# Performance work log

Measured on AMD Instinct MI355X. Metric: run time of the kernel, lower is better.

The kernel has to match this reference:

```python
import jax, jax.numpy as jnp
import numpy as np

N_NODES = 50000
N_EDGES = 1600000
DIM = 128
HEADS = 8
HEAD_DIM = DIM // HEADS


def setup_inputs() -> dict:
    key = jax.random.key(0)
    ks = jax.random.split(key, 12)
    s = 1.0 / np.sqrt(DIM)
    return {
        "x": jax.random.normal(ks[0], (N_NODES, DIM), dtype=jnp.float32),
        "src": jax.random.randint(ks[1], (N_EDGES,), 0, N_NODES, dtype=jnp.int32),
        "dst": jax.random.randint(ks[2], (N_EDGES,), 0, N_NODES, dtype=jnp.int32),
        "Wq": jax.random.uniform(ks[3], (DIM, DIM), jnp.float32, -s, s),
        "bq": jax.random.uniform(ks[4], (DIM,), jnp.float32, -s, s),
        "Wk": jax.random.uniform(ks[5], (DIM, DIM), jnp.float32, -s, s),
        "bk": jax.random.uniform(ks[6], (DIM,), jnp.float32, -s, s),
        "Wv": jax.random.uniform(ks[7], (DIM, DIM), jnp.float32, -s, s),
        "bv": jax.random.uniform(ks[8], (DIM,), jnp.float32, -s, s),
        "Wo": jax.random.uniform(ks[9], (DIM, DIM), jnp.float32, -s, s),
        "bo": jax.random.uniform(ks[10], (DIM,), jnp.float32, -s, s),
    }


def reference(x, src, dst, Wq, bq, Wk, bk, Wv, bv, Wo, bo):
    # Linear projections (torch Linear: x @ W.T + b), split into heads
    q = (x @ Wq.T + bq).reshape(-1, HEADS, HEAD_DIM)  # [N, H, Dh]
    k = (x @ Wk.T + bk).reshape(-1, HEADS, HEAD_DIM)
    v = (x @ Wv.T + bv).reshape(-1, HEADS, HEAD_DIM)

    # u_dot_v: per-edge dot of q[src] and k[dst] per head -> [E, H]
    scores = jnp.einsum("ehd,ehd->eh", q[src], k[dst]) / np.sqrt(HEAD_DIM).astype(np.float32)

    # edge_softmax: softmax over edges grouped by destination node
    m = jax.ops.segment_max(scores, dst, num_segments=N_NODES)  # [N, H]
    e = jnp.exp(scores - m[dst])
    z = jax.ops.segment_sum(e, dst, num_segments=N_NODES)  # [N, H]
    probs = e / z[dst]  # [E, H]

    # u_mul_e_sum: scatter-add of v[src] * probs into dst -> [N, H, Dh]
    msg = v[src] * probs[:, :, None]
    agg = jax.ops.segment_sum(msg, dst, num_segments=N_NODES)

    out = agg.reshape(-1, DIM) @ Wo.T + bo  # dropout p=0.0 -> identity
    return out
```

## Files before the change

### kernel.cpp

```cpp
#include <hip/hip_runtime.h>
#include <hip/hip_bf16.h>
#include <math.h>

#define N_NODES 50000
#define N_EDGES 1600000
#define NBUCK 256
#define NBUCK_ACTIVE ((N_NODES + 255) / 256)
#define P1_BLOCKS ((N_EDGES + 4095) / 4096)
#define CAP 9216
#define QKV_BLOCKS ((N_NODES + 63) / 64)

typedef short bf16x8 __attribute__((ext_vector_type(8)));
typedef float f32x4 __attribute__((ext_vector_type(4)));

#define SC2 0.3606737602222409f
#define MNEG -1.0e30f

static __device__ __forceinline__ unsigned short f2bf(float f) {
  unsigned int b = __float_as_uint(f);
  unsigned int r = (b + 0x7FFFu + ((b >> 16) & 1u)) >> 16;
  return (unsigned short)r;
}
static __device__ __forceinline__ float bf_lo(unsigned int u) {
  return __uint_as_float(u << 16);
}
static __device__ __forceinline__ float bf_hi(unsigned int u) {
  return __uint_as_float(u & 0xFFFF0000u);
}

__global__ __launch_bounds__(256) void bucket_partition(
    const int* __restrict__ src, const int* __restrict__ dst,
    int* __restrict__ bcursor, unsigned int* __restrict__ packed,
    const float* __restrict__ Wq, const float* __restrict__ Wk,
    const float* __restrict__ Wv, const float* __restrict__ Wo,
    unsigned short* __restrict__ wb) {
  const int t = threadIdx.x;
  if (blockIdx.x < 64) {
    int idx = blockIdx.x * 256 + t;
    wb[idx] = f2bf(Wq[idx]);
    wb[16384 + idx] = f2bf(Wk[idx]);
    wb[32768 + idx] = f2bf(Wv[idx]);
    wb[49152 + idx] = f2bf(Wo[idx]);
  }

  __shared__ int h[NBUCK];
  __shared__ int sd[NBUCK];
  __shared__ int lofs[NBUCK];
  __shared__ int gbase[NBUCK];
  __shared__ unsigned int stage[4096];
  __shared__ unsigned short sbin[4096];

  h[t] = 0;
  __syncthreads();
  const int ebase = blockIdx.x * 4096;
  const int count = min(4096, N_EDGES - ebase);
  const int base4 = blockIdx.x * 1024;
  unsigned int val[16];
  int binrank[16];
#pragma unroll
  for (int i = 0; i < 4; ++i) {
    int i4 = base4 + i * 256 + t;
    if (i4 < N_EDGES / 4) {
      int4 s4 = ((const int4*)src)[i4];
      int4 d4 = ((const int4*)dst)[i4];
      int ss[4] = {s4.x, s4.y, s4.z, s4.w};
      int dd[4] = {d4.x, d4.y, d4.z, d4.w};
#pragma unroll
      for (int j = 0; j < 4; ++j) {
        val[i * 4 + j] = ((unsigned)dd[j] << 16) | (unsigned)ss[j];
        int bin = dd[j] >> 8;
        int r = atomicAdd(&h[bin], 1);
        binrank[i * 4 + j] = (bin << 16) | r;
      }
    } else {
#pragma unroll
      for (int j = 0; j < 4; ++j) binrank[i * 4 + j] = -1;
    }
  }
  __syncthreads();
  const int own = h[t];
  if (own > 0) gbase[t] = atomicAdd(&bcursor[t], own);
  sd[t] = own;
  __syncthreads();
  for (int d = 1; d < NBUCK; d <<= 1) {
    int v = (t >= d) ? sd[t - d] : 0;
    __syncthreads();
    sd[t] += v;
    __syncthreads();
  }
  lofs[t] = sd[t] - own;
  __syncthreads();
#pragma unroll
  for (int i = 0; i < 16; ++i) {
    if (binrank[i] >= 0) {
      int bin = binrank[i] >> 16;
      int r = binrank[i] & 0xFFFF;
      int slot = lofs[bin] + r;
      stage[slot] = val[i];
      sbin[slot] = (unsigned short)bin;
    }
  }
  __syncthreads();
  for (int j = t; j < count; j += 256) {
    int b = sbin[j];
    packed[(size_t)b * CAP + gbase[b] + (j - lofs[b])] = stage[j];
  }
}

__global__ __launch_bounds__(256) void qkv_and_finalize(
    const float* __restrict__ x, const unsigned short* __restrict__ wb,
    const float* __restrict__ bq, const float* __restrict__ bk,
    const float* __restrict__ bv,
    unsigned short* __restrict__ qrec, unsigned short* __restrict__ kb,
    unsigned short* __restrict__ vrec,
    const unsigned int* __restrict__ packed, const int* __restrict__ bcursor,
    int* __restrict__ ebeg, int* __restrict__ eend,
    unsigned short* __restrict__ ssrc, int nrows) {
  __shared__ __align__(16) unsigned short sbuf[64 * 136];
  const int tid = threadIdx.x;

  if (blockIdx.x < QKV_BLOCKS) {
    const int w = tid >> 6;
    const int lane = tid & 63;
    const int lr = lane & 15;
    const int kg = lane >> 4;
    const int rowbase = blockIdx.x * 64;
    const int arow = min(rowbase + w * 16 + lr, nrows - 1);

    bf16x8 af[4];
    const float* xr = x + (size_t)arow * 128;
#pragma unroll
    for (int ksub = 0; ksub < 4; ++ksub) {
      const int k0 = ksub * 32 + kg * 8;
      float4 f0 = *(const float4*)(xr + k0);
      float4 f1 = *(const float4*)(xr + k0 + 4);
      af[ksub][0] = (short)f2bf(f0.x);
      af[ksub][1] = (short)f2bf(f0.y);
      af[ksub][2] = (short)f2bf(f0.z);
      af[ksub][3] = (short)f2bf(f0.w);
      af[ksub][4] = (short)f2bf(f1.x);
      af[ksub][5] = (short)f2bf(f1.y);
      af[ksub][6] = (short)f2bf(f1.z);
      af[ksub][7] = (short)f2bf(f1.w);
    }

    for (int p = 0; p < 3; ++p) {
      const unsigned short* wp = wb + p * 16384;
      const float* bias = (p == 0) ? bq : (p == 1) ? bk : bv;
      unsigned short* gout = (p == 0) ? qrec : (p == 1) ? kb : vrec;
      f32x4 acc[8];
#pragma unroll
      for (int nt = 0; nt < 8; ++nt) {
        float b = bias[nt * 16 + lr];
        acc[nt] = (f32x4){b, b, b, b};
      }
#pragma unroll
      for (int ksub = 0; ksub < 4; ++ksub) {
#pragma unroll
        for (int nt = 0; nt < 8; ++nt) {
          bf16x8 bfr = *(const bf16x8*)(wp + (size_t)(nt * 16 + lr) * 128 +
                                        ksub * 32 + kg * 8);
          acc[nt] = __builtin_amdgcn_mfma_f32_16x16x32_bf16(af[ksub], bfr,
                                                            acc[nt], 0, 0, 0);
        }
      }
      __syncthreads();
#pragma unroll
      for (int nt = 0; nt < 8; ++nt) {
        int col = nt * 16 + lr;
#pragma unroll
        for (int r = 0; r < 4; ++r)
          sbuf[(w * 16 + kg * 4 + r) * 136 + col] = f2bf(acc[nt][r]);
      }
      __syncthreads();
#pragma unroll
      for (int i = 0; i < 4; ++i) {
        int idx = i * 256 + tid;
        int lrow = idx >> 4;
        int u16o = (idx & 15) * 8;
        int grow = rowbase + lrow;
        if (grow < nrows)
          *(uint4*)(gout + (size_t)grow * 128 + u16o) =
              *(const uint4*)&sbuf[lrow * 136 + u16o];
      }
    }
  } else {
    int* cnt = (int*)sbuf;
    int* sd = cnt + NBUCK;
    int* cur = sd + NBUCK;
    const int t = tid;
    const int b = blockIdx.x - QKV_BLOCKS;
    const int beg = b * CAP;
    const int n_in_bucket = min(bcursor[b], CAP);
    cnt[t] = 0;
    __syncthreads();
    for (int e = t; e < n_in_bucket; e += 256)
      atomicAdd(&cnt[(packed[beg + e] >> 16) & 255], 1);
    __syncthreads();
    const int own = cnt[t];
    sd[t] = own;
    __syncthreads();
    for (int d = 1; d < NBUCK; d <<= 1) {
      int v = (t >= d) ? sd[t - d] : 0;
      __syncthreads();
      sd[t] += v;
      __syncthreads();
    }
    const int excl = sd[t] - own;
    cur[t] = excl;
    const int node = b * 256 + t;
    if (node < N_NODES) {
      ebeg[node] = beg + excl;
      eend[node] = beg + excl + own;
    }
    __syncthreads();
    for (int e = t; e < n_in_bucket; e += 256) {
      unsigned int p = packed[beg + e];
      int local = (p >> 16) & 255;
      int r = atomicAdd(&cur[local], 1);
      ssrc[beg + r] = (unsigned short)(p & 0xFFFFu);
    }
  }
}

__global__ __launch_bounds__(256, 4) void edge_agg_out(
    const unsigned short* __restrict__ qrec, const unsigned short* __restrict__ vrec,
    const unsigned short* __restrict__ kb,
    const int* __restrict__ ebeg, const int* __restrict__ eend,
    const unsigned short* __restrict__ ssrc,
    const unsigned short* __restrict__ wo, const float* __restrict__ bo,
    float* __restrict__ out) {
  __shared__ __align__(16) unsigned short aggs[16 * 136];
  const int wid = threadIdx.x >> 6;
  const int lane = threadIdx.x & 63;
  const int l16 = lane & 15;
  const int qq = lane >> 4;
  const int loff = l16 * 8;
  const int nbase = blockIdx.x * 16;

#define DOT8(t0)                                                       \
  (bf_lo(t0.x) * k0 + bf_hi(t0.x) * k1 + bf_lo(t0.y) * k2 +            \
   bf_hi(t0.y) * k3 + bf_lo(t0.z) * k4 + bf_hi(t0.z) * k5 +            \
   bf_lo(t0.w) * k6 + bf_hi(t0.w) * k7)

#define ACC8(pe, tv)                        \
  a0 = fmaf(pe, bf_lo(tv.x), a0);           \
  a1 = fmaf(pe, bf_hi(tv.x), a1);           \
  a2 = fmaf(pe, bf_lo(tv.y), a2);           \
  a3 = fmaf(pe, bf_hi(tv.y), a3);           \
  a4 = fmaf(pe, bf_lo(tv.z), a4);           \
  a5 = fmaf(pe, bf_hi(tv.z), a5);           \
  a6 = fmaf(pe, bf_lo(tv.w), a6);           \
  a7 = fmaf(pe, bf_hi(tv.w), a7)

  for (int i = 0; i < 4; ++i) {
    const int n = nbase + wid * 4 + i;
    const uint4 ku = *(const uint4*)(kb + (size_t)n * 128 + loff);
    const float k0 = bf_lo(ku.x), k1 = bf_hi(ku.x);
    const float k2 = bf_lo(ku.y), k3 = bf_hi(ku.y);
    const float k4 = bf_lo(ku.z), k5 = bf_hi(ku.z);
    const float k6 = bf_lo(ku.w), k7 = bf_hi(ku.w);

    const int start = ebeg[n];
    const int end = eend[n];

    float zz = 0.0f;
    float a0 = 0, a1 = 0, a2 = 0, a3 = 0, a4 = 0, a5 = 0, a6 = 0, a7 = 0;

    int base = start;
    for (; base + 16 <= end; base += 16) {
      int sA = ssrc[base + qq];
      int sB = ssrc[base + 4 + qq];
      int sC = ssrc[base + 8 + qq];
      int sD = ssrc[base + 12 + qq];
      const uint4 qA = *(const uint4*)(qrec + ((size_t)sA << 7) + loff);
      const uint4 vA = *(const uint4*)(vrec + ((size_t)sA << 7) + loff);
      const uint4 qB = *(const uint4*)(qrec + ((size_t)sB << 7) + loff);
      const uint4 vB = *(const uint4*)(vrec + ((size_t)sB << 7) + loff);
      const uint4 qC = *(const uint4*)(qrec + ((size_t)sC << 7) + loff);
      const uint4 vC = *(const uint4*)(vrec + ((size_t)sC << 7) + loff);
      const uint4 qD = *(const uint4*)(qrec + ((size_t)sD << 7) + loff);
      const uint4 vD = *(const uint4*)(vrec + ((size_t)sD << 7) + loff);

      float pA = DOT8(qA);
      float pB = DOT8(qB);
      float pC = DOT8(qC);
      float pD = DOT8(qD);
      pA += __shfl_xor(pA, 1);
      pB += __shfl_xor(pB, 1);
      pC += __shfl_xor(pC, 1);
      pD += __shfl_xor(pD, 1);
      float peA = __builtin_amdgcn_exp2f(pA * SC2);
      float peB = __builtin_amdgcn_exp2f(pB * SC2);
      float peC = __builtin_amdgcn_exp2f(pC * SC2);
      float peD = __builtin_amdgcn_exp2f(pD * SC2);
      zz += (peA + peB) + (peC + peD);
      ACC8(peA, vA);
      ACC8(peB, vB);
      ACC8(peC, vC);
      ACC8(peD, vD);
    }
    for (; base < end; base += 4) {
      int idx = base + qq;
      bool valid = idx < end;
      int s = ssrc[valid ? idx : end - 1];
      const uint4 q0 = *(const uint4*)(qrec + ((size_t)s << 7) + loff);
      const uint4 v0 = *(const uint4*)(vrec + ((size_t)s << 7) + loff);
      float p = DOT8(q0);
      p += __shfl_xor(p, 1);
      float pe = __builtin_amdgcn_exp2f(valid ? p * SC2 : MNEG);
      zz += pe;
      ACC8(pe, v0);
    }

#pragma unroll
    for (int off = 16; off <= 32; off <<= 1) {
      zz += __shfl_xor(zz, off);
      a0 += __shfl_xor(a0, off);
      a1 += __shfl_xor(a1, off);
      a2 += __shfl_xor(a2, off);
      a3 += __shfl_xor(a3, off);
      a4 += __shfl_xor(a4, off);
      a5 += __shfl_xor(a5, off);
      a6 += __shfl_xor(a6, off);
      a7 += __shfl_xor(a7, off);
    }
    float inv = (zz > 0.0f) ? 1.0f / zz : 0.0f;

    if (qq == 0) {
      unsigned short o[8] = {f2bf(a0 * inv), f2bf(a1 * inv), f2bf(a2 * inv),
                             f2bf(a3 * inv), f2bf(a4 * inv), f2bf(a5 * inv),
                             f2bf(a6 * inv), f2bf(a7 * inv)};
      *(uint4*)&aggs[(wid * 4 + i) * 136 + loff] = *(const uint4*)o;
    }
  }
#undef DOT8
#undef ACC8

  __syncthreads();

  bf16x8 af[4];
#pragma unroll
  for (int ksub = 0; ksub < 4; ++ksub)
    af[ksub] = *(const bf16x8*)&aggs[l16 * 136 + ksub * 32 + qq * 8];

  f32x4 acc[2];
#pragma unroll
  for (int j = 0; j < 2; ++j) {
    int nt = wid * 2 + j;
    float b = bo[nt * 16 + l16];
    acc[j] = (f32x4){b, b, b, b};
  }
#pragma unroll
  for (int ksub = 0; ksub < 4; ++ksub) {
#pragma unroll
    for (int j = 0; j < 2; ++j) {
      int nt = wid * 2 + j;
      bf16x8 bfr = *(const bf16x8*)(wo + (size_t)(nt * 16 + l16) * 128 +
                                    ksub * 32 + qq * 8);
      acc[j] =
          __builtin_amdgcn_mfma_f32_16x16x32_bf16(af[ksub], bfr, acc[j], 0, 0, 0);
    }
  }
#pragma unroll
  for (int j = 0; j < 2; ++j) {
    int col = (wid * 2 + j) * 16 + l16;
#pragma unroll
    for (int r = 0; r < 4; ++r) {
      int grow = nbase + qq * 4 + r;
      out[(size_t)grow * 128 + col] = acc[j][r];
    }
  }
}

extern "C" void kernel_launch(void* const* d_in, const int* in_sizes, int n_in,
                              void* d_out, int out_size, void* d_ws, size_t ws_size,
                              hipStream_t stream) {
  const float* x  = (const float*)d_in[0];
  const int* src  = (const int*)d_in[1];
  const int* dst  = (const int*)d_in[2];
  const float* Wq = (const float*)d_in[3];
  const float* bq = (const float*)d_in[4];
  const float* Wk = (const float*)d_in[5];
  const float* bk = (const float*)d_in[6];
  const float* Wv = (const float*)d_in[7];
  const float* bv = (const float*)d_in[8];
  const float* Wo = (const float*)d_in[9];
  const float* bo = (const float*)d_in[10];
  float* out = (float*)d_out;

  char* ws = (char*)d_ws;
  size_t off = 0;
  auto carve = [&](size_t bytes) {
    size_t r = off;
    off = (off + bytes + 255) & ~(size_t)255;
    return r;
  };
  unsigned short* qrec = (unsigned short*)(ws + carve((size_t)N_NODES * 256));
  unsigned short* vrec = (unsigned short*)(ws + carve((size_t)N_NODES * 256));
  unsigned short* kb   = (unsigned short*)(ws + carve((size_t)N_NODES * 256));
  unsigned int* packed = (unsigned int*)(ws + carve((size_t)NBUCK * CAP * 4));
  unsigned short* ssrc = (unsigned short*)(ws + carve((size_t)NBUCK * CAP * 2));
  int* ebeg    = (int*)(ws + carve((size_t)N_NODES * sizeof(int)));
  int* eend    = (int*)(ws + carve((size_t)N_NODES * sizeof(int)));
  int* bcursor = (int*)(ws + carve(NBUCK * sizeof(int)));
  unsigned short* wb = (unsigned short*)(ws + carve((size_t)4 * 128 * 128 * 2));

  hipMemsetAsync(bcursor, 0, NBUCK * sizeof(int), stream);

  bucket_partition<<<P1_BLOCKS, 256, 0, stream>>>(src, dst, bcursor, packed,
                                                  Wq, Wk, Wv, Wo, wb);

  qkv_and_finalize<<<QKV_BLOCKS + NBUCK_ACTIVE, 256, 0, stream>>>(
      x, wb, bq, bk, bv, qrec, kb, vrec, packed, bcursor, ebeg, eend, ssrc,
      N_NODES);

  edge_agg_out<<<N_NODES / 16, 256, 0, stream>>>(qrec, vrec, kb, ebeg, eend,
                                                 ssrc, wb + 3 * 16384, bo, out);
}
```

Before: 191.5 us.

## Co-schedule QKV projection with edge bucketing; split bucket finalize into own kernel

Moves the edge bucket partition into the same launch as the QKV projection, so the projection blocks and partition blocks run concurrently. The bucket finalize stage becomes a separate small kernel. The QKV blocks now read the fp32 weights directly and convert them to bf16 on the fly, removing the dependency on a pre-converted weight buffer; only Wo is still pre-converted. The cost is redundant weight conversion in every QKV block, more fp32 weight loads, and larger shared memory for the combined kernel.

```diff
diff --git a/kernel.cpp b/kernel.cpp
--- a/kernel.cpp
+++ b/kernel.cpp
@@ -27,99 +27,33 @@
 static __device__ __forceinline__ float bf_hi(unsigned int u) {
   return __uint_as_float(u & 0xFFFF0000u);
 }
-
-__global__ __launch_bounds__(256) void bucket_partition(
+static __device__ __forceinline__ bf16x8 cvt8(const float* p) {
+  float4 w0 = *(const float4*)p;
+  float4 w1 = *(const float4*)(p + 4);
+  bf16x8 r;
+  r[0] = (short)f2bf(w0.x); r[1] = (short)f2bf(w0.y);
+  r[2] = (short)f2bf(w0.z); r[3] = (short)f2bf(w0.w);
+  r[4] = (short)f2bf(w1.x); r[5] = (short)f2bf(w1.y);
+  r[6] = (short)f2bf(w1.z); r[7] = (short)f2bf(w1.w);
+  return r;
+}
+
+__global__ __launch_bounds__(256) void qkv_and_partition(
+    const float* __restrict__ x,
+    const float* __restrict__ Wq, const float* __restrict__ bq,
+    const float* __restrict__ Wk, const float* __restrict__ bk,
+    const float* __restrict__ Wv, const float* __restrict__ bv,
+    const float* __restrict__ Wo,
+    unsigned short* __restrict__ qrec, unsigned short* __restrict__ kb,
+    unsigned short* __restrict__ vrec,
     const int* __restrict__ src, const int* __restrict__ dst,
     int* __restrict__ bcursor, unsigned int* __restrict__ packed,
-    const float* __restrict__ Wq, const float* __restrict__ Wk,
-    const float* __restrict__ Wv, const float* __restrict__ Wo,
-    unsigned short* __restrict__ wb) {
-  const int t = threadIdx.x;
-  if (blockIdx.x < 64) {
-    int idx = blockIdx.x * 256 + t;
-    wb[idx] = f2bf(Wq[idx]);
-    wb[16384 + idx] = f2bf(Wk[idx]);
-    wb[32768 + idx] = f2bf(Wv[idx]);
-    wb[49152 + idx] = f2bf(Wo[idx]);
-  }
-
-  __shared__ int h[NBUCK];
-  __shared__ int sd[NBUCK];
-  __shared__ int lofs[NBUCK];
-  __shared__ int gbase[NBUCK];
-  __shared__ unsigned int stage[4096];
-  __shared__ unsigned short sbin[4096];
-
-  h[t] = 0;
-  __syncthreads();
-  const int ebase = blockIdx.x * 4096;
-  const int count = min(4096, N_EDGES - ebase);
-  const int base4 = blockIdx.x * 1024;
-  unsigned int val[16];
-  int binrank[16];
-#pragma unroll
-  for (int i = 0; i < 4; ++i) {
-    int i4 = base4 + i * 256 + t;
-    if (i4 < N_EDGES / 4) {
-      int4 s4 = ((const int4*)src)[i4];
-      int4 d4 = ((const int4*)dst)[i4];
-      int ss[4] = {s4.x, s4.y, s4.z, s4.w};
-      int dd[4] = {d4.x, d4.y, d4.z, d4.w};
-#pragma unroll
-      for (int j = 0; j < 4; ++j) {
-        val[i * 4 + j] = ((unsigned)dd[j] << 16) | (unsigned)ss[j];
-        int bin = dd[j] >> 8;
-        int r = atomicAdd(&h[bin], 1);
-        binrank[i * 4 + j] = (bin << 16) | r;
-      }
-    } else {
-#pragma unroll
-      for (int j = 0; j < 4; ++j) binrank[i * 4 + j] = -1;
-    }
-  }
-  __syncthreads();
-  const int own = h[t];
-  if (own > 0) gbase[t] = atomicAdd(&bcursor[t], own);
-  sd[t] = own;
-  __syncthreads();
-  for (int d = 1; d < NBUCK; d <<= 1) {
-    int v = (t >= d) ? sd[t - d] : 0;
-    __syncthreads();
-    sd[t] += v;
-    __syncthreads();
-  }
-  lofs[t] = sd[t] - own;
-  __syncthreads();
-#pragma unroll
-  for (int i = 0; i < 16; ++i) {
-    if (binrank[i] >= 0) {
-      int bin = binrank[i] >> 16;
-      int r = binrank[i] & 0xFFFF;
-      int slot = lofs[bin] + r;
-      stage[slot] = val[i];
-      sbin[slot] = (unsigned short)bin;
-    }
-  }
-  __syncthreads();
-  for (int j = t; j < count; j += 256) {
-    int b = sbin[j];
-    packed[(size_t)b * CAP + gbase[b] + (j - lofs[b])] = stage[j];
-  }
-}
-
-__global__ __launch_bounds__(256) void qkv_and_finalize(
-    const float* __restrict__ x, const unsigned short* __restrict__ wb,
-    const float* __restrict__ bq, const float* __restrict__ bk,
-    const float* __restrict__ bv,
-    unsigned short* __restrict__ qrec, unsigned short* __restrict__ kb,
-    unsigned short* __restrict__ vrec,
-    const unsigned int* __restrict__ packed, const int* __restrict__ bcursor,
-    int* __restrict__ ebeg, int* __restrict__ eend,
-    unsigned short* __restrict__ ssrc, int nrows) {
-  __shared__ __align__(16) unsigned short sbuf[64 * 136];
+    unsigned short* __restrict__ wb, int nrows) {
+  __shared__ __align__(16) unsigned char smem[28672];
   const int tid = threadIdx.x;
 
   if (blockIdx.x < QKV_BLOCKS) {
+    unsigned short* sbuf = (unsigned short*)smem;
     const int w = tid >> 6;
     const int lane = tid & 63;
     const int lr = lane & 15;
@@ -130,22 +64,11 @@
     bf16x8 af[4];
     const float* xr = x + (size_t)arow * 128;
 #pragma unroll
-    for (int ksub = 0; ksub < 4; ++ksub) {
-      const int k0 = ksub * 32 + kg * 8;
-      float4 f0 = *(const float4*)(xr + k0);
-      float4 f1 = *(const float4*)(xr + k0 + 4);
-      af[ksub][0] = (short)f2bf(f0.x);
-      af[ksub][1] = (short)f2bf(f0.y);
-      af[ksub][2] = (short)f2bf(f0.z);
-      af[ksub][3] = (short)f2bf(f0.w);
-      af[ksub][4] = (short)f2bf(f1.x);
-      af[ksub][5] = (short)f2bf(f1.y);
-      af[ksub][6] = (short)f2bf(f1.z);
-      af[ksub][7] = (short)f2bf(f1.w);
-    }
+    for (int ksub = 0; ksub < 4; ++ksub)
+      af[ksub] = cvt8(xr + ksub * 32 + kg * 8);
 
     for (int p = 0; p < 3; ++p) {
-      const unsigned short* wp = wb + p * 16384;
+      const float* W = (p == 0) ? Wq : (p == 1) ? Wk : Wv;
       const float* bias = (p == 0) ? bq : (p == 1) ? bk : bv;
       unsigned short* gout = (p == 0) ? qrec : (p == 1) ? kb : vrec;
       f32x4 acc[8];
@@ -158,8 +81,7 @@
       for (int ksub = 0; ksub < 4; ++ksub) {
 #pragma unroll
         for (int nt = 0; nt < 8; ++nt) {
-          bf16x8 bfr = *(const bf16x8*)(wp + (size_t)(nt * 16 + lr) * 128 +
-                                        ksub * 32 + kg * 8);
+          bf16x8 bfr = cvt8(W + (size_t)(nt * 16 + lr) * 128 + ksub * 32 + kg * 8);
           acc[nt] = __builtin_amdgcn_mfma_f32_16x16x32_bf16(af[ksub], bfr,
                                                             acc[nt], 0, 0, 0);
         }
@@ -185,19 +107,49 @@
       }
     }
   } else {
-    int* cnt = (int*)sbuf;
-    int* sd = cnt + NBUCK;
-    int* cur = sd + NBUCK;
+    const int pb = blockIdx.x - QKV_BLOCKS;
+    if (pb < 64) {
+      int idx = pb * 256 + tid;
+      wb[idx] = f2bf(Wo[idx]);
+    }
+    int* h = (int*)smem;
+    int* sd = h + NBUCK;
+    int* lofs = sd + NBUCK;
+    int* gbase = lofs + NBUCK;
+    unsigned int* stage = (unsigned int*)(gbase + NBUCK);
+    unsigned short* sbin = (unsigned short*)(stage + 4096);
+
     const int t = tid;
-    const int b = blockIdx.x - QKV_BLOCKS;
-    const int beg = b * CAP;
-    const int n_in_bucket = min(bcursor[b], CAP);
-    cnt[t] = 0;
-    __syncthreads();
-    for (int e = t; e < n_in_bucket; e += 256)
-      atomicAdd(&cnt[(packed[beg + e] >> 16) & 255], 1);
-    __syncthreads();
-    const int own = cnt[t];
+    h[t] = 0;
+    __syncthreads();
+    const int ebase = pb * 4096;
+    const int count = min(4096, N_EDGES - ebase);
+    const int base4 = pb * 1024;
+    unsigned int val[16];
+    int binrank[16];
+#pragma unroll
+    for (int i = 0; i < 4; ++i) {
+      int i4 = base4 + i * 256 + t;
+      if (i4 < N_EDGES / 4) {
+        int4 s4 = ((const int4*)src)[i4];
+        int4 d4 = ((const int4*)dst)[i4];
+        int ss[4] = {s4.x, s4.y, s4.z, s4.w};
+        int dd[4] = {d4.x, d4.y, d4.z, d4.w};
+#pragma unroll
+        for (int j = 0; j < 4; ++j) {
+          val[i * 4 + j] = ((unsigned)dd[j] << 16) | (unsigned)ss[j];
+          int bin = dd[j] >> 8;
+          int r = atomicAdd(&h[bin], 1);
+          binrank[i * 4 + j] = (bin << 16) | r;
+        }
+      } else {
+#pragma unroll
+        for (int j = 0; j < 4; ++j) binrank[i * 4 + j] = -1;
+      }
+    }
+    __syncthreads();
+    const int own = h[t];
+    if (own > 0) gbase[t] = atomicAdd(&bcursor[t], own);
     sd[t] = own;
     __syncthreads();
     for (int d = 1; d < NBUCK; d <<= 1) {
@@ -206,20 +158,64 @@
       sd[t] += v;
       __syncthreads();
     }
-    const int excl = sd[t] - own;
-    cur[t] = excl;
-    const int node = b * 256 + t;
-    if (node < N_NODES) {
-      ebeg[node] = beg + excl;
-      eend[node] = beg + excl + own;
-    }
-    __syncthreads();
-    for (int e = t; e < n_in_bucket; e += 256) {
-      unsigned int p = packed[beg + e];
-      int local = (p >> 16) & 255;
-      int r = atomicAdd(&cur[local], 1);
-      ssrc[beg + r] = (unsigned short)(p & 0xFFFFu);
-    }
+    lofs[t] = sd[t] - own;
+    __syncthreads();
+#pragma unroll
+    for (int i = 0; i < 16; ++i) {
+      if (binrank[i] >= 0) {
+        int bin = binrank[i] >> 16;
+        int r = binrank[i] & 0xFFFF;
+        int slot = lofs[bin] + r;
+        stage[slot] = val[i];
+        sbin[slot] = (unsigned short)bin;
+      }
+    }
+    __syncthreads();
+    for (int j = t; j < count; j += 256) {
+      int b = sbin[j];
+      packed[(size_t)b * CAP + gbase[b] + (j - lofs[b])] = stage[j];
+    }
+  }
+}
+
+__global__ __launch_bounds__(256) void bucket_finalize(
+    const unsigned int* __restrict__ packed, const int* __restrict__ bcursor,
+    int* __restrict__ ebeg, int* __restrict__ eend,
+    unsigned short* __restrict__ ssrc) {
+  __shared__ int cnt[NBUCK];
+  __shared__ int sd[NBUCK];
+  __shared__ int cur[NBUCK];
+  const int t = threadIdx.x;
+  const int b = blockIdx.x;
+  const int beg = b * CAP;
+  const int n_in_bucket = min(bcursor[b], CAP);
+  cnt[t] = 0;
+  __syncthreads();
+  for (int e = t; e < n_in_bucket; e += 256)
+    atomicAdd(&cnt[(packed[beg + e] >> 16) & 255], 1);
+  __syncthreads();
+  const int own = cnt[t];
+  sd[t] = own;
+  __syncthreads();
+  for (int d = 1; d < NBUCK; d <<= 1) {
+    int v = (t >= d) ? sd[t - d] : 0;
+    __syncthreads();
+    sd[t] += v;
+    __syncthreads();
+  }
+  const int excl = sd[t] - own;
+  cur[t] = excl;
+  const int node = b * 256 + t;
+  if (node < N_NODES) {
+    ebeg[node] = beg + excl;
+    eend[node] = beg + excl + own;
+  }
+  __syncthreads();
+  for (int e = t; e < n_in_bucket; e += 256) {
+    unsigned int p = packed[beg + e];
+    int local = (p >> 16) & 255;
+    int r = atomicAdd(&cur[local], 1);
+    ssrc[beg + r] = (unsigned short)(p & 0xFFFFu);
   }
 }
 
@@ -404,17 +400,17 @@
   int* ebeg    = (int*)(ws + carve((size_t)N_NODES * sizeof(int)));
   int* eend    = (int*)(ws + carve((size_t)N_NODES * sizeof(int)));
   int* bcursor = (int*)(ws + carve(NBUCK * sizeof(int)));
-  unsigned short* wb = (unsigned short*)(ws + carve((size_t)4 * 128 * 128 * 2));
+  unsigned short* wb = (unsigned short*)(ws + carve((size_t)128 * 128 * 2));
 
   hipMemsetAsync(bcursor, 0, NBUCK * sizeof(int), stream);
 
-  bucket_partition<<<P1_BLOCKS, 256, 0, stream>>>(src, dst, bcursor, packed,
-                                                  Wq, Wk, Wv, Wo, wb);
-
-  qkv_and_finalize<<<QKV_BLOCKS + NBUCK_ACTIVE, 256, 0, stream>>>(
-      x, wb, bq, bk, bv, qrec, kb, vrec, packed, bcursor, ebeg, eend, ssrc,
-      N_NODES);
+  qkv_and_partition<<<QKV_BLOCKS + P1_BLOCKS, 256, 0, stream>>>(
+      x, Wq, bq, Wk, bk, Wv, bv, Wo, qrec, kb, vrec, src, dst, bcursor,
+      packed, wb, N_NODES);
+
+  bucket_finalize<<<NBUCK_ACTIVE, 256, 0, stream>>>(packed, bcursor, ebeg,
+                                                    eend, ssrc);
 
   edge_agg_out<<<N_NODES / 16, 256, 0, stream>>>(qrec, vrec, kb, ebeg, eend,
-                                                 ssrc, wb + 3 * 16384, bo, out);
-}
+                                                 ssrc, wb, bo, out);
+}
```

After: 240.1 us. 1.25x slower.

## Co-schedule QKV projection with edge bucket partition and split finalize kernel

Applied to the files above, without the earlier changes.

Moves the weight bf16 conversion and bcursor zeroing into a small init kernel, replacing the memset. The bucket partition now runs in the same launch as the QKV GEMM blocks, so both proceed concurrently. Bucket finalization becomes its own kernel. This trades a memset plus one launch for an extra small kernel, and the combined kernel needs a larger shared-memory footprint (28 KB), which may lower occupancy for the GEMM blocks.

```diff
diff --git a/kernel.cpp b/kernel.cpp
--- a/kernel.cpp
+++ b/kernel.cpp
@@ -28,98 +28,32 @@
   return __uint_as_float(u & 0xFFFF0000u);
 }
 
-__global__ __launch_bounds__(256) void bucket_partition(
-    const int* __restrict__ src, const int* __restrict__ dst,
-    int* __restrict__ bcursor, unsigned int* __restrict__ packed,
+__global__ __launch_bounds__(256) void init_kernel(
     const float* __restrict__ Wq, const float* __restrict__ Wk,
     const float* __restrict__ Wv, const float* __restrict__ Wo,
-    unsigned short* __restrict__ wb) {
+    unsigned short* __restrict__ wb, int* __restrict__ bcursor) {
   const int t = threadIdx.x;
-  if (blockIdx.x < 64) {
-    int idx = blockIdx.x * 256 + t;
-    wb[idx] = f2bf(Wq[idx]);
-    wb[16384 + idx] = f2bf(Wk[idx]);
-    wb[32768 + idx] = f2bf(Wv[idx]);
-    wb[49152 + idx] = f2bf(Wo[idx]);
-  }
-
-  __shared__ int h[NBUCK];
-  __shared__ int sd[NBUCK];
-  __shared__ int lofs[NBUCK];
-  __shared__ int gbase[NBUCK];
-  __shared__ unsigned int stage[4096];
-  __shared__ unsigned short sbin[4096];
-
-  h[t] = 0;
-  __syncthreads();
-  const int ebase = blockIdx.x * 4096;
-  const int count = min(4096, N_EDGES - ebase);
-  const int base4 = blockIdx.x * 1024;
-  unsigned int val[16];
-  int binrank[16];
-#pragma unroll
-  for (int i = 0; i < 4; ++i) {
-    int i4 = base4 + i * 256 + t;
-    if (i4 < N_EDGES / 4) {
-      int4 s4 = ((const int4*)src)[i4];
-      int4 d4 = ((const int4*)dst)[i4];
-      int ss[4] = {s4.x, s4.y, s4.z, s4.w};
-      int dd[4] = {d4.x, d4.y, d4.z, d4.w};
-#pragma unroll
-      for (int j = 0; j < 4; ++j) {
-        val[i * 4 + j] = ((unsigned)dd[j] << 16) | (unsigned)ss[j];
-        int bin = dd[j] >> 8;
-        int r = atomicAdd(&h[bin], 1);
-        binrank[i * 4 + j] = (bin << 16) | r;
-      }
-    } else {
-#pragma unroll
-      for (int j = 0; j < 4; ++j) binrank[i * 4 + j] = -1;
-    }
-  }
-  __syncthreads();
-  const int own = h[t];
-  if (own > 0) gbase[t] = atomicAdd(&bcursor[t], own);
-  sd[t] = own;
-  __syncthreads();
-  for (int d = 1; d < NBUCK; d <<= 1) {
-    int v = (t >= d) ? sd[t - d] : 0;
-    __syncthreads();
-    sd[t] += v;
-    __syncthreads();
-  }
-  lofs[t] = sd[t] - own;
-  __syncthreads();
-#pragma unroll
-  for (int i = 0; i < 16; ++i) {
-    if (binrank[i] >= 0) {
-      int bin = binrank[i] >> 16;
-      int r = binrank[i] & 0xFFFF;
-      int slot = lofs[bin] + r;
-      stage[slot] = val[i];
-      sbin[slot] = (unsigned short)bin;
-    }
-  }
-  __syncthreads();
-  for (int j = t; j < count; j += 256) {
-    int b = sbin[j];
-    packed[(size_t)b * CAP + gbase[b] + (j - lofs[b])] = stage[j];
-  }
-}
-
-__global__ __launch_bounds__(256) void qkv_and_finalize(
+  int idx = blockIdx.x * 256 + t;
+  wb[idx] = f2bf(Wq[idx]);
+  wb[16384 + idx] = f2bf(Wk[idx]);
+  wb[32768 + idx] = f2bf(Wv[idx]);
+  wb[49152 + idx] = f2bf(Wo[idx]);
+  if (blockIdx.x == 0) bcursor[t] = 0;
+}
+
+__global__ __launch_bounds__(256) void qkv_and_partition(
     const float* __restrict__ x, const unsigned short* __restrict__ wb,
     const float* __restrict__ bq, const float* __restrict__ bk,
     const float* __restrict__ bv,
     unsigned short* __restrict__ qrec, unsigned short* __restrict__ kb,
     unsigned short* __restrict__ vrec,
-    const unsigned int* __restrict__ packed, const int* __restrict__ bcursor,
-    int* __restrict__ ebeg, int* __restrict__ eend,
-    unsigned short* __restrict__ ssrc, int nrows) {
-  __shared__ __align__(16) unsigned short sbuf[64 * 136];
+    const int* __restrict__ src, const int* __restrict__ dst,
+    int* __restrict__ bcursor, unsigned int* __restrict__ packed, int nrows) {
+  __shared__ __align__(16) unsigned char smem[28672];
   const int tid = threadIdx.x;
 
   if (blockIdx.x < QKV_BLOCKS) {
+    unsigned short* sbuf = (unsigned short*)smem;
     const int w = tid >> 6;
     const int lane = tid & 63;
     const int lr = lane & 15;
@@ -185,19 +119,45 @@
       }
     }
   } else {
-    int* cnt = (int*)sbuf;
-    int* sd = cnt + NBUCK;
-    int* cur = sd + NBUCK;
+    const int pb = blockIdx.x - QKV_BLOCKS;
+    int* h = (int*)smem;
+    int* sd = h + NBUCK;
+    int* lofs = sd + NBUCK;
+    int* gbase = lofs + NBUCK;
+    unsigned int* stage = (unsigned int*)(gbase + NBUCK);
+    unsigned short* sbin = (unsigned short*)(stage + 4096);
+
     const int t = tid;
-    const int b = blockIdx.x - QKV_BLOCKS;
-    const int beg = b * CAP;
-    const int n_in_bucket = min(bcursor[b], CAP);
-    cnt[t] = 0;
-    __syncthreads();
-    for (int e = t; e < n_in_bucket; e += 256)
-      atomicAdd(&cnt[(packed[beg + e] >> 16) & 255], 1);
-    __syncthreads();
-    const int own = cnt[t];
+    h[t] = 0;
+    __syncthreads();
+    const int ebase = pb * 4096;
+    const int count = min(4096, N_EDGES - ebase);
+    const int base4 = pb * 1024;
+    unsigned int val[16];
+    int binrank[16];
+#pragma unroll
+    for (int i = 0; i < 4; ++i) {
+      int i4 = base4 + i * 256 + t;
+      if (i4 < N_EDGES / 4) {
+        int4 s4 = ((const int4*)src)[i4];
+        int4 d4 = ((const int4*)dst)[i4];
+        int ss[4] = {s4.x, s4.y, s4.z, s4.w};
+        int dd[4] = {d4.x, d4.y, d4.z, d4.w};
+#pragma unroll
+        for (int j = 0; j < 4; ++j) {
+          val[i * 4 + j] = ((unsigned)dd[j] << 16) | (unsigned)ss[j];
+          int bin = dd[j] >> 8;
+          int r = atomicAdd(&h[bin], 1);
+          binrank[i * 4 + j] = (bin << 16) | r;
+        }
+      } else {
+#pragma unroll
+        for (int j = 0; j < 4; ++j) binrank[i * 4 + j] = -1;
+      }
+    }
+    __syncthreads();
+    const int own = h[t];
+    if (own > 0) gbase[t] = atomicAdd(&bcursor[t], own);
     sd[t] = own;
     __syncthreads();
     for (int d = 1; d < NBUCK; d <<= 1) {
@@ -206,20 +166,64 @@
       sd[t] += v;
       __syncthreads();
     }
-    const int excl = sd[t] - own;
-    cur[t] = excl;
-    const int node = b * 256 + t;
-    if (node < N_NODES) {
-      ebeg[node] = beg + excl;
-      eend[node] = beg + excl + own;
-    }
-    __syncthreads();
-    for (int e = t; e < n_in_bucket; e += 256) {
-      unsigned int p = packed[beg + e];
-      int local = (p >> 16) & 255;
-      int r = atomicAdd(&cur[local], 1);
-      ssrc[beg + r] = (unsigned short)(p & 0xFFFFu);
-    }
+    lofs[t] = sd[t] - own;
+    __syncthreads();
+#pragma unroll
+    for (int i = 0; i < 16; ++i) {
+      if (binrank[i] >= 0) {
+        int bin = binrank[i] >> 16;
+        int r = binrank[i] & 0xFFFF;
+        int slot = lofs[bin] + r;
+        stage[slot] = val[i];
+        sbin[slot] = (unsigned short)bin;
+      }
+    }
+    __syncthreads();
+    for (int j = t; j < count; j += 256) {
+      int b = sbin[j];
+      packed[(size_t)b * CAP + gbase[b] + (j - lofs[b])] = stage[j];
+    }
+  }
+}
+
+__global__ __launch_bounds__(256) void bucket_finalize(
+    const unsigned int* __restrict__ packed, const int* __restrict__ bcursor,
+    int* __restrict__ ebeg, int* __restrict__ eend,
+    unsigned short* __restrict__ ssrc) {
+  __shared__ int cnt[NBUCK];
+  __shared__ int sd[NBUCK];
+  __shared__ int cur[NBUCK];
+  const int t = threadIdx.x;
+  const int b = blockIdx.x;
+  const int beg = b * CAP;
+  const int n_in_bucket = min(bcursor[b], CAP);
+  cnt[t] = 0;
+  __syncthreads();
+  for (int e = t; e < n_in_bucket; e += 256)
+    atomicAdd(&cnt[(packed[beg + e] >> 16) & 255], 1);
+  __syncthreads();
+  const int own = cnt[t];
+  sd[t] = own;
+  __syncthreads();
+  for (int d = 1; d < NBUCK; d <<= 1) {
+    int v = (t >= d) ? sd[t - d] : 0;
+    __syncthreads();
+    sd[t] += v;
+    __syncthreads();
+  }
+  const int excl = sd[t] - own;
+  cur[t] = excl;
+  const int node = b * 256 + t;
+  if (node < N_NODES) {
+    ebeg[node] = beg + excl;
+    eend[node] = beg + excl + own;
+  }
+  __syncthreads();
+  for (int e = t; e < n_in_bucket; e += 256) {
+    unsigned int p = packed[beg + e];
+    int local = (p >> 16) & 255;
+    int r = atomicAdd(&cur[local], 1);
+    ssrc[beg + r] = (unsigned short)(p & 0xFFFFu);
   }
 }
 
@@ -406,14 +410,13 @@
   int* bcursor = (int*)(ws + carve(NBUCK * sizeof(int)));
   unsigned short* wb = (unsigned short*)(ws + carve((size_t)4 * 128 * 128 * 2));
 
-  hipMemsetAsync(bcursor, 0, NBUCK * sizeof(int), stream);
-
-  bucket_partition<<<P1_BLOCKS, 256, 0, stream>>>(src, dst, bcursor, packed,
-                                                  Wq, Wk, Wv, Wo, wb);
-
-  qkv_and_finalize<<<QKV_BLOCKS + NBUCK_ACTIVE, 256, 0, stream>>>(
-      x, wb, bq, bk, bv, qrec, kb, vrec, packed, bcursor, ebeg, eend, ssrc,
-      N_NODES);
+  init_kernel<<<64, 256, 0, stream>>>(Wq, Wk, Wv, Wo, wb, bcursor);
+
+  qkv_and_partition<<<QKV_BLOCKS + P1_BLOCKS, 256, 0, stream>>>(
+      x, wb, bq, bk, bv, qrec, kb, vrec, src, dst, bcursor, packed, N_NODES);
+
+  bucket_finalize<<<NBUCK_ACTIVE, 256, 0, stream>>>(packed, bcursor, ebeg,
+                                                    eend, ssrc);
 
   edge_agg_out<<<N_NODES / 16, 256, 0, stream>>>(qrec, vrec, kb, ebeg, eend,
                                                  ssrc, wb + 3 * 16384, bo, out);
```

Result: slower. 199.7 us (+4.3%).
